# Performance work log

Hardware: AMD Instinct MI355X
Metric: run time of the kernel (lower is better)

Reference implementation:

```python
import jax, jax.numpy as jnp
import numpy as np

NC = 80          # num classes
NL = 3           # num levels
NA = 3           # anchors per level
MAX_DET = 25     # self.maxdetnum
IOU_THRES = 0.7
MAX_WH = 7680.0  # class offset for class-aware NMS (agnostic=False)


def _xywh2xyxy(b):
    cx, cy, w, h = b[..., 0], b[..., 1], b[..., 2], b[..., 3]
    return jnp.stack((cx - w / 2, cy - h / 2, cx + w / 2, cy + h / 2), -1)


def _decode(xi, anchors_i):
    # xi: (bs, na, ny, nx, nc+5) raw logits -> (bs, na*ny*nx, nc+7)
    bs, na, ny, nx, _ = xi.shape
    y = jax.nn.sigmoid(xi)
    yv, xv = jnp.meshgrid(jnp.arange(ny, dtype=xi.dtype),
                          jnp.arange(nx, dtype=xi.dtype), indexing='ij')
    pos = jnp.stack((xv, yv), -1)                    # (ny, nx, 2): (x_col, y_row) grid coords
    xy = y[..., :2] * 2 + (pos - 0.5)                # grid = pos - 0.5 (as in source: xy*2 + grid)
    wh = (y[..., 2:4] * 2) ** 2 * anchors_i[None, :, None, None, :]
    conf = y[..., 4:]                                # obj + nc class probs
    posb = jnp.broadcast_to(pos, xy.shape)
    out = jnp.concatenate((xy, wh, conf, posb), -1)  # (bs, na, ny, nx, nc+7)
    return out.reshape(bs, -1, out.shape[-1])


def _iou_one_vs_all(box, boxes):
    # xyxy IoU of one box vs (N,4) boxes
    lt = jnp.maximum(box[:2], boxes[:, :2])
    rb = jnp.minimum(box[2:], boxes[:, 2:])
    wh = jnp.clip(rb - lt, 0.0)
    inter = wh[:, 0] * wh[:, 1]
    area1 = (box[2] - box[0]) * (box[3] - box[1])
    area2 = (boxes[:, 2] - boxes[:, 0]) * (boxes[:, 3] - boxes[:, 1])
    return inter / (area1 + area2 - inter)


def _nms_image(pred):
    # pred: (N, nc+7). Note: source computes xc = conf>0.25 but never applies it.
    obj = pred[:, 4]
    cls = pred[:, 5:5 + NC] * obj[:, None]           # x[:,5:-2] *= x[:,4:5]
    box = _xywh2xyxy(pred[:, :4])
    conf = cls.max(axis=1)
    j = jnp.argmax(cls, axis=1).astype(pred.dtype)
    det = jnp.concatenate((box, conf[:, None], j[:, None], pred[:, -2:]), axis=1)  # (N, 8)
    order = jnp.argsort(-conf)                       # score-descending (N < max_nms=30000 so cap is no-op)
    det = det[order]
    boxes = det[:, :4] + det[:, 5:6] * MAX_WH        # class-offset boxes
    n = det.shape[0]

    def body(k, carry):
        valid, sel, selv = carry
        has = valid.any()
        idx = jnp.argmax(valid)                      # first unsuppressed = highest remaining score
        iou = _iou_one_vs_all(boxes[idx], boxes)
        valid = valid & (iou <= IOU_THRES)           # self-IoU = 1 > thres removes idx from pool
        sel = sel.at[k].set(idx)
        selv = selv.at[k].set(has)
        return valid, sel, selv

    valid0 = jnp.ones((n,), bool)
    sel0 = jnp.zeros((MAX_DET,), jnp.int32)
    selv0 = jnp.zeros((MAX_DET,), bool)
    _, sel, selv = jax.lax.fori_loop(0, MAX_DET, body, (valid0, sel0, selv0))
    out = det[sel] * selv[:, None].astype(det.dtype)  # pad invalid slots with zeros
    return out, selv


def _level(feature, xi, anchors_i):
    pred = _decode(xi, anchors_i)                    # (bs, N, nc+7)
    dets, selv = jax.vmap(_nms_image)(pred)          # (bs, MAX_DET, 8), (bs, MAX_DET)
    fmap = jnp.transpose(feature, (0, 2, 3, 1))      # (bs, ny, nx, C)
    row = dets[:, :, 7].astype(jnp.int32)            # det[:, -1] = y grid coord -> posX in source
    col = dets[:, :, 6].astype(jnp.int32)            # det[:, -2] = x grid coord -> posY in source
    gathered = jax.vmap(lambda f, r, c: f[r, c])(fmap, row, col)  # (bs, MAX_DET, C)
    return gathered * selv[:, :, None].astype(fmap.dtype)         # rows beyond n_det stay zero


def setup_inputs() -> dict:
    key = jax.random.key(0)
    ks = jax.random.split(key, 7)
    bs = 16
    grids = [(80, 80), (40, 40), (20, 20)]
    chans = [128, 256, 512]
    inp = {}
    for i, ((ny, nx), c) in enumerate(zip(grids, chans)):
        inp[f"x{i}"] = jax.random.normal(ks[i], (bs, NA, ny, nx, NC + 5), jnp.float32)
        inp[f"features{i}"] = jax.random.normal(ks[3 + i], (bs, c, ny, nx), jnp.float32)
    inp["anchors"] = jax.random.uniform(ks[6], (NL, NA, 2), jnp.float32, 1.0, 6.0)
    return inp


def reference(features0, features1, features2, x0, x1, x2, anchors):
    feats = (features0, features1, features2)
    xs = (x0, x1, x2)
    return tuple(_level(feats[i], xs[i], anchors[i]) for i in range(NL))
```

## Files before the change

kernel.cpp:

```cpp
#include <hip/hip_runtime.h>
#include <math.h>
#include <float.h>

#define MAX_DET 25
#define IOU_THRES 0.7f
#define MAX_WH 7680.0f
#define TOPK 256
#define MCAP 512

__device__ __forceinline__ float sigm(float v) {
#pragma clang fp contract(off)
    return 1.0f / (1.0f + expf(-v));
}

__global__ __launch_bounds__(256) void decode_all_kernel(
    const float* __restrict__ x0, const float* __restrict__ x1, const float* __restrict__ x2,
    float* __restrict__ confW, unsigned short* __restrict__ bcW)
{
#pragma clang fp contract(off)
    int t = blockIdx.x * 256 + threadIdx.x;
    int g = t >> 2;
    int l4 = t & 3;
    const float* row;
    if (g < 307200)       row = x0 + (long)g * 85;
    else if (g < 384000)  row = x1 + (long)(g - 307200) * 85;
    else                  row = x2 + (long)(g - 384000) * 85;

    float bv = -FLT_MAX; int bc = 0;
#pragma unroll
    for (int j = 0; j < 20; ++j) {
        float v = row[5 + l4 + 4 * j];
        if (v > bv) { bv = v; bc = l4 + 4 * j; }
    }
#pragma unroll
    for (int off = 2; off; off >>= 1) {
        float ov = __shfl_xor(bv, off);
        int   oc = __shfl_xor(bc, off);
        if (ov > bv || (ov == bv && oc < bc)) { bv = ov; bc = oc; }
    }
    if (l4 != 0) return;

    float v4 = row[4];
    confW[g] = sigm(bv) * sigm(v4);
    bcW[g] = (unsigned short)bc;
}

struct LvlParams {
    const float* feat;
    const float* x;
    long candOff;
    long outOff;
    int C;
};

template<int NY, int NX>
__device__ __forceinline__ void run_group(
    const float* __restrict__ gconf, const unsigned short* __restrict__ gbc,
    const float* __restrict__ xg, const float* __restrict__ anch,
    const float* __restrict__ feat, int C, long outOff, int b,
    float* sconf, unsigned long long* sk, unsigned* hists, float (*sbox)[4],
    int* selIdx, int* selValid, unsigned* wtot , unsigned* misc ,
    float* __restrict__ out)
{
#pragma clang fp contract(off)
    constexpr int HW = NY * NX;
    constexpr int NPC = 3 * HW;
    const int tid = threadIdx.x;
    const int lane = tid & 63;
    const int wid = tid >> 6;

    const float4* gc4 = (const float4*)gconf;
    float4* sc4 = (float4*)sconf;
    for (int i = tid; i < NPC / 4; i += 1024) sc4[i] = gc4[i];
    if (tid < MAX_DET) selValid[tid] = 0;
    if (tid == 0) misc[0] = 0;

    unsigned B = 0, B2 = 0, K2 = 0;
    for (int pass = 0; pass < 2; ++pass) {
        for (int i = tid; i < 4096; i += 1024) hists[i] = 0;
        __syncthreads();
        for (int i = tid; i < NPC; i += 1024) {
            unsigned bits = __float_as_uint(sconf[i]);
            if (pass == 0) atomicAdd(&hists[((tid & 1) << 11) + (bits >> 19)], 1u);
            else if ((bits >> 19) == B) atomicAdd(&hists[((tid & 1) << 11) + ((bits >> 8) & 2047u)], 1u);
        }
        __syncthreads();
        unsigned part = hists[2 * tid] + hists[2 * tid + 1]
                      + hists[2048 + 2 * tid] + hists[2048 + 2 * tid + 1];
        unsigned s = part;
#pragma unroll
        for (int d = 1; d < 64; d <<= 1) {
            unsigned v = __shfl_down(s, d);
            if (lane < 64 - d) s += v;
        }
        if (lane == 0) wtot[wid] = s;
        __syncthreads();
        unsigned S = s;
        for (int w = wid + 1; w < 16; ++w) S += wtot[w];
        unsigned Ktgt = (pass == 0) ? TOPK : K2;
        if (S >= Ktgt && S - part < Ktgt) {
            unsigned acc = S - part;
            for (int i = 1; i >= 0; --i) {
                int bin = 2 * tid + i;
                unsigned h = hists[bin] + hists[2048 + bin];
                acc += h;
                if (acc >= Ktgt) { misc[2] = (unsigned)bin; misc[3] = acc - h; break; }
            }
        }
        __syncthreads();
        if (pass == 0) { B = misc[2]; K2 = Ktgt - misc[3]; }
        else           { B2 = misc[2]; }
        __syncthreads();
    }
    unsigned T = (B << 19) | (B2 << 8);

    for (int i = tid; i < NPC; i += 1024) {
        unsigned bits = __float_as_uint(sconf[i]);
        if (bits >= T) {
            unsigned pos = atomicAdd(&misc[0], 1u);
            if (pos < MCAP)
                sk[pos] = ((unsigned long long)bits << 32) | (unsigned)(~i);
        }
    }
    __syncthreads();
    unsigned cn = misc[0];
    int n = (cn < (unsigned)MCAP) ? (int)cn : MCAP;

    for (int i = tid; i < n; i += 1024) {
        int idx = (int)(~(unsigned)sk[i]);
        const float* row = xg + (long)idx * 85;
        float v0 = row[0], v1 = row[1], v2 = row[2], v3 = row[3];
        int bc = (int)gbc[idx];
        int a   = idx / HW;
        int rem = idx - a * HW;
        int gy  = rem / NX;
        int gx  = rem - gy * NX;

        float cx = sigm(v0) * 2.0f + ((float)gx - 0.5f);
        float cy = sigm(v1) * 2.0f + ((float)gy - 0.5f);
        float tw = sigm(v2) * 2.0f, th = sigm(v3) * 2.0f;
        float w = (tw * tw) * anch[a * 2 + 0];
        float h = (th * th) * anch[a * 2 + 1];
        float x1 = cx - w / 2.0f, y1 = cy - h / 2.0f;
        float x2 = cx + w / 2.0f, y2 = cy + h / 2.0f;
        float offc = (float)bc * MAX_WH;
        sbox[i][0] = x1 + offc; sbox[i][1] = y1 + offc;
        sbox[i][2] = x2 + offc; sbox[i][3] = y2 + offc;
    }
    __syncthreads();

    if (tid < 64) {
        unsigned long long kreg[8];
#pragma unroll
        for (int j = 0; j < 8; ++j) {
            int s = tid + 64 * j;
            kreg[j] = (s < n) ? sk[s] : 0ULL;
        }
        float ex1 = 0.f, ey1 = 0.f, ex2 = 0.f, ey2 = 0.f;
        int k = 0;
        while (k < MAX_DET) {
            unsigned long long mk = kreg[0]; int ms = tid;
#pragma unroll
            for (int j = 1; j < 8; ++j)
                if (kreg[j] > mk) { mk = kreg[j]; ms = tid + 64 * j; }
#pragma unroll
            for (int off = 32; off; off >>= 1) {
                unsigned long long ok = __shfl_xor(mk, off);
                int os = __shfl_xor(ms, off);
                if (ok > mk) { mk = ok; ms = os; }
            }
            if (mk == 0ULL) break;
#pragma unroll
            for (int j = 0; j < 8; ++j)
                if (ms == tid + 64 * j) kreg[j] = 0ULL;

            float cx1 = sbox[ms][0], cy1 = sbox[ms][1];
            float cx2 = sbox[ms][2], cy2 = sbox[ms][3];
            bool rej = false;
            if (tid < k) {
                float ltx = fmaxf(ex1, cx1), lty = fmaxf(ey1, cy1);
                float rbx = fminf(ex2, cx2), rby = fminf(ey2, cy2);
                float ww = fmaxf(rbx - ltx, 0.0f), hh = fmaxf(rby - lty, 0.0f);
                float inter = ww * hh;
                float area1 = (ex2 - ex1) * (ey2 - ey1);
                float area2 = (cx2 - cx1) * (cy2 - cy1);
                float iou = inter / (area1 + area2 - inter);
                rej = iou > IOU_THRES;
            }
            rej = __any(rej);
            if (!rej) {
                if (tid == k) { ex1 = cx1; ey1 = cy1; ex2 = cx2; ey2 = cy2; }
                if (tid == 0) { selIdx[k] = (int)(~(unsigned)mk); selValid[k] = 1; }
                ++k;
            }
        }
    }
    __syncthreads();

    const float* fb = feat + (long)b * C * HW;
    long obase = outOff + (long)b * MAX_DET * C;
    for (int e = tid; e < MAX_DET * C; e += 1024) {
        int k2 = e / C, c = e - k2 * C;
        float val = 0.0f;
        if (selValid[k2]) {
            int idx = selIdx[k2];
            int rem = idx % HW;
            val = fb[(long)c * HW + rem];
        }
        out[obase + e] = val;
    }
}

__global__ __launch_bounds__(1024) void select_nms_gather_kernel(
    const float* __restrict__ confW, const unsigned short* __restrict__ bcW,
    const float* __restrict__ anch, float* __restrict__ out,
    LvlParams p0, LvlParams p1, LvlParams p2)
{
    __shared__ float sconf[19200];
    __shared__ unsigned long long sk[MCAP];
    __shared__ unsigned hists[4096];
    __shared__ float sbox[MCAP][4];
    __shared__ int   selIdx[MAX_DET];
    __shared__ int   selValid[MAX_DET];
    __shared__ unsigned wtot[16];
    __shared__ unsigned misc[4];

    int grp = blockIdx.x;
    int lvl = grp >> 4, b = grp & 15;
    if (lvl == 0) {
        long base = p0.candOff + (long)b * 19200;
        run_group<80, 80>(confW + base, bcW + base, p0.x + base * 85, anch + 0,
                          p0.feat, p0.C, p0.outOff, b,
                          sconf, sk, hists, sbox, selIdx, selValid, wtot, misc, out);
    } else if (lvl == 1) {
        long base = p1.candOff + (long)b * 4800;
        run_group<40, 40>(confW + base, bcW + base, p1.x + (long)b * 4800 * 85, anch + 6,
                          p1.feat, p1.C, p1.outOff, b,
                          sconf, sk, hists, sbox, selIdx, selValid, wtot, misc, out);
    } else {
        long base = p2.candOff + (long)b * 1200;
        run_group<20, 20>(confW + base, bcW + base, p2.x + (long)b * 1200 * 85, anch + 12,
                          p2.feat, p2.C, p2.outOff, b,
                          sconf, sk, hists, sbox, selIdx, selValid, wtot, misc, out);
    }
}

extern "C" void kernel_launch(void* const* d_in, const int* in_sizes, int n_in,
                              void* d_out, int out_size, void* d_ws, size_t ws_size,
                              hipStream_t stream)
{
    const float* xs[3] = {nullptr, nullptr, nullptr};
    const float* fs[3] = {nullptr, nullptr, nullptr};
    const float* anch  = nullptr;
    for (int i = 0; i < n_in; ++i) {
        const float* p = (const float*)d_in[i];
        switch (in_sizes[i]) {
            case 26112000: xs[0] = p; break;
            case 6528000:  xs[1] = p; break;
            case 1632000:  xs[2] = p; break;
            case 13107200: fs[0] = p; break;
            case 6553600:  fs[1] = p; break;
            case 3276800:  fs[2] = p; break;
            case 18:       anch  = p; break;
        }
    }

    char* wsb = (char*)d_ws;
    float*          confW = (float*)wsb;
    unsigned short* bcW   = (unsigned short*)(wsb + 1612800L);

    decode_all_kernel<<<6300, 256, 0, stream>>>(xs[0], xs[1], xs[2], confW, bcW);

    LvlParams P0{fs[0], xs[0] - 0L,        0L,      0L,      128};
    LvlParams P1{fs[1], xs[1],             307200L, 51200L,  256};
    LvlParams P2{fs[2], xs[2],             384000L, 153600L, 512};

    select_nms_gather_kernel<<<48, 1024, 0, stream>>>(confW, bcW, anch, (float*)d_out, P0, P1, P2);
}
```

Baseline: 61.25 us.

## Fuse first histogram pass into conf copy and use 2 lanes per decode row

The decode kernel now uses two threads per anchor row instead of four, each scanning 40 class logits, with a single shuffle to combine and half as many blocks. In the selection kernel, the first radix-histogram pass is built while the confidence values are copied into shared memory, which removes a separate sweep over shared memory and one barrier. Fewer threads per row lowers parallelism and memory-level concurrency in the decode, and the fused histogram adds atomics to the copy loop.

```diff
diff --git a/kernel.cpp b/kernel.cpp
--- a/kernel.cpp
+++ b/kernel.cpp
@@ -19,8 +19,8 @@
 {
 #pragma clang fp contract(off)
     int t = blockIdx.x * 256 + threadIdx.x;
-    int g = t >> 2;
-    int l4 = t & 3;
+    int g = t >> 1;
+    int l2 = t & 1;
     const float* row;
     if (g < 307200)       row = x0 + (long)g * 85;
     else if (g < 384000)  row = x1 + (long)(g - 307200) * 85;
@@ -28,17 +28,16 @@
 
     float bv = -FLT_MAX; int bc = 0;
 #pragma unroll
-    for (int j = 0; j < 20; ++j) {
-        float v = row[5 + l4 + 4 * j];
-        if (v > bv) { bv = v; bc = l4 + 4 * j; }
-    }
-#pragma unroll
-    for (int off = 2; off; off >>= 1) {
-        float ov = __shfl_xor(bv, off);
-        int   oc = __shfl_xor(bc, off);
+    for (int j = 0; j < 40; ++j) {
+        float v = row[5 + l2 + 2 * j];
+        if (v > bv) { bv = v; bc = l2 + 2 * j; }
+    }
+    {
+        float ov = __shfl_xor(bv, 1);
+        int   oc = __shfl_xor(bc, 1);
         if (ov > bv || (ov == bv && oc < bc)) { bv = ov; bc = oc; }
     }
-    if (l4 != 0) return;
+    if (l2 != 0) return;
 
     float v4 = row[4];
     confW[g] = sigm(bv) * sigm(v4);
@@ -69,22 +68,37 @@
     const int lane = tid & 63;
     const int wid = tid >> 6;
 
+    if (tid < MAX_DET) selValid[tid] = 0;
+    if (tid == 0) misc[0] = 0;
+    for (int i = tid; i < 4096; i += 1024) hists[i] = 0;
+    __syncthreads();
+
     const float4* gc4 = (const float4*)gconf;
     float4* sc4 = (float4*)sconf;
-    for (int i = tid; i < NPC / 4; i += 1024) sc4[i] = gc4[i];
-    if (tid < MAX_DET) selValid[tid] = 0;
-    if (tid == 0) misc[0] = 0;
+    const int sh = (tid & 1) << 11;
+    for (int i = tid; i < NPC / 4; i += 1024) {
+        float4 v = gc4[i];
+        sc4[i] = v;
+        atomicAdd(&hists[sh + (__float_as_uint(v.x) >> 19)], 1u);
+        atomicAdd(&hists[sh + (__float_as_uint(v.y) >> 19)], 1u);
+        atomicAdd(&hists[sh + (__float_as_uint(v.z) >> 19)], 1u);
+        atomicAdd(&hists[sh + (__float_as_uint(v.w) >> 19)], 1u);
+    }
+    __syncthreads();
 
     unsigned B = 0, B2 = 0, K2 = 0;
     for (int pass = 0; pass < 2; ++pass) {
-        for (int i = tid; i < 4096; i += 1024) hists[i] = 0;
-        __syncthreads();
-        for (int i = tid; i < NPC; i += 1024) {
-            unsigned bits = __float_as_uint(sconf[i]);
-            if (pass == 0) atomicAdd(&hists[((tid & 1) << 11) + (bits >> 19)], 1u);
-            else if ((bits >> 19) == B) atomicAdd(&hists[((tid & 1) << 11) + ((bits >> 8) & 2047u)], 1u);
-        }
-        __syncthreads();
+        if (pass == 1) {
+            __syncthreads();
+            for (int i = tid; i < 4096; i += 1024) hists[i] = 0;
+            __syncthreads();
+            for (int i = tid; i < NPC; i += 1024) {
+                unsigned bits = __float_as_uint(sconf[i]);
+                if ((bits >> 19) == B)
+                    atomicAdd(&hists[sh + ((bits >> 8) & 2047u)], 1u);
+            }
+            __syncthreads();
+        }
         unsigned part = hists[2 * tid] + hists[2 * tid + 1]
                       + hists[2048 + 2 * tid] + hists[2048 + 2 * tid + 1];
         unsigned s = part;
@@ -110,7 +124,6 @@
         __syncthreads();
         if (pass == 0) { B = misc[2]; K2 = Ktgt - misc[3]; }
         else           { B2 = misc[2]; }
-        __syncthreads();
     }
     unsigned T = (B << 19) | (B2 << 8);
 
@@ -269,11 +282,11 @@
     float*          confW = (float*)wsb;
     unsigned short* bcW   = (unsigned short*)(wsb + 1612800L);
 
-    decode_all_kernel<<<6300, 256, 0, stream>>>(xs[0], xs[1], xs[2], confW, bcW);
-
-    LvlParams P0{fs[0], xs[0] - 0L,        0L,      0L,      128};
-    LvlParams P1{fs[1], xs[1],             307200L, 51200L,  256};
-    LvlParams P2{fs[2], xs[2],             384000L, 153600L, 512};
+    decode_all_kernel<<<3150, 256, 0, stream>>>(xs[0], xs[1], xs[2], confW, bcW);
+
+    LvlParams P0{fs[0], xs[0], 0L,      0L,      128};
+    LvlParams P1{fs[1], xs[1], 307200L, 51200L,  256};
+    LvlParams P2{fs[2], xs[2], 384000L, 153600L, 512};
 
     select_nms_gather_kernel<<<48, 1024, 0, stream>>>(confW, bcW, anch, (float*)d_out, P0, P1, P2);
 }
```

Measured after the change: 75.09 us. +22.6%, slower.
